# Kernel tuning notes

Measured on AMD Instinct MI355X. Metric: run time of the kernel, lower is better.

The kernel has to match this reference:

```python
import jax, jax.numpy as jnp
import numpy as np

N = 100000       # nodes
E = 3200000      # edges (avg degree 32)
C_IN = 32        # input_channels


def _glorot(key, shape):
    lim = float(np.sqrt(6.0 / (shape[0] + shape[1])))
    return jax.random.uniform(key, shape, jnp.float32, -lim, lim)


def setup_inputs() -> dict:
    key = jax.random.key(0)
    ks = jax.random.split(key, 8)
    x = jax.random.normal(ks[0], (N, C_IN), jnp.float32)
    edge_index = jax.random.randint(ks[1], (2, E), 0, N, dtype=jnp.int64)
    return {
        "x": x,
        "edge_index": edge_index,
        "W1": _glorot(ks[2], (C_IN, 16)), "b1": jnp.zeros((16,), jnp.float32),
        "W2": _glorot(ks[3], (16, 32)),   "b2": jnp.zeros((32,), jnp.float32),
        "W3": _glorot(ks[4], (32, 16)),   "b3": jnp.zeros((16,), jnp.float32),
        "Wfc": _glorot(ks[5], (16, 1)),   "bfc": jnp.zeros((1,), jnp.float32),
    }


def _gcn_conv(x, W, b, src, dst, norm, n):
    # PyG GCNConv: transform then degree-normalized scatter-add (self-loops in src/dst)
    h = x @ W                              # [N, out]
    m = h[src] * norm[:, None]             # gather + per-edge scale
    return jax.ops.segment_sum(m, dst, num_segments=n) + b


def reference(x, edge_index, W1, b1, W2, b2, W3, b3, Wfc, bfc):
    n = x.shape[0]
    loops = jnp.arange(n, dtype=edge_index.dtype)
    src = jnp.concatenate([edge_index[0], loops])   # add self-loops
    dst = jnp.concatenate([edge_index[1], loops])
    deg = jax.ops.segment_sum(jnp.ones(src.shape[0], x.dtype), dst, num_segments=n)
    dis = jnp.where(deg > 0, jax.lax.rsqrt(deg), jnp.zeros((), x.dtype))
    norm = dis[src] * dis[dst]                      # symmetric D^-1/2 A D^-1/2

    h = jax.nn.relu(_gcn_conv(x, W1, b1, src, dst, norm, n))
    h = jax.nn.relu(_gcn_conv(h, W2, b2, src, dst, norm, n))
    h = jax.nn.relu(_gcn_conv(h, W3, b3, src, dst, norm, n))
    out = h @ Wfc + bfc                             # [N, 1]
    return jnp.mean(out)
```

## Files before the change

### kernel.cpp

```cpp
#include <hip/hip_runtime.h>

static constexpr int BLK = 256;
static constexpr int CHUNK = 4096;
static constexpr int BSHIFT = 7;
static constexpr int BNODES = 128;
static constexpr int MAXNB = 1024;

typedef unsigned short bf16t;

__device__ __forceinline__ float bf_lo(unsigned u) { return __uint_as_float(u << 16); }
__device__ __forceinline__ float bf_hi(unsigned u) { return __uint_as_float(u & 0xFFFF0000u); }
__device__ __forceinline__ unsigned bf_r(float f) {
    unsigned x = __float_as_uint(f);
    x += 0x7fffu + ((x >> 16) & 1u);
    return x >> 16;
}
__device__ __forceinline__ unsigned bf_pack(float lo, float hi) {
    return bf_r(lo) | (bf_r(hi) << 16);
}


__global__ __launch_bounds__(BLK) void k_hist(const int* __restrict__ dst, int* __restrict__ ghist,
                                              int e, int NB, int NBLK) {
    __shared__ int h[MAXNB];
    for (int i = threadIdx.x; i < NB; i += BLK) h[i] = 0;
    __syncthreads();
    int base = blockIdx.x * CHUNK;
    int lim = min(e - base, CHUNK);
    for (int r = threadIdx.x; r < lim; r += BLK) atomicAdd(&h[dst[base + r] >> BSHIFT], 1);
    __syncthreads();
    for (int b = threadIdx.x; b < NB; b += BLK) ghist[b * NBLK + blockIdx.x] = h[b];
}

__global__ void k_scan1(const int* __restrict__ in, int* __restrict__ excl,
                        int* __restrict__ partials, int n) {
    __shared__ int s[BLK];
    int i = blockIdx.x * BLK + threadIdx.x;
    int v = (i < n) ? in[i] : 0;
    s[threadIdx.x] = v;
    __syncthreads();
    for (int off = 1; off < BLK; off <<= 1) {
        int t = ((int)threadIdx.x >= off) ? s[threadIdx.x - off] : 0;
        __syncthreads();
        s[threadIdx.x] += t;
        __syncthreads();
    }
    if (i < n) excl[i] = s[threadIdx.x] - v;
    if (threadIdx.x == BLK - 1) partials[blockIdx.x] = s[BLK - 1];
}

__global__ void k_scan2(int* __restrict__ partials, int P) {
    __shared__ int s[1024];
    int carry = 0;
    for (int base = 0; base < P; base += 1024) {
        int i = base + (int)threadIdx.x;
        int v = (i < P) ? partials[i] : 0;
        s[threadIdx.x] = v;
        __syncthreads();
        for (int off = 1; off < 1024; off <<= 1) {
            int t = ((int)threadIdx.x >= off) ? s[threadIdx.x - off] : 0;
            __syncthreads();
            s[threadIdx.x] += t;
            __syncthreads();
        }
        if (i < P) partials[i] = carry + s[threadIdx.x] - v;
        carry += s[1023];
        __syncthreads();
    }
}

__global__ void k_scan3(int* __restrict__ excl, const int* __restrict__ partials, int n) {
    int i = blockIdx.x * BLK + threadIdx.x;
    if (i < n) excl[i] += partials[blockIdx.x];
}

__global__ __launch_bounds__(BLK) void k_bin(const int* __restrict__ src, const int* __restrict__ dst,
                                             const int* __restrict__ goff, unsigned int* __restrict__ keys,
                                             int e, int NB, int NBLK) {
    __shared__ int hcur[MAXNB];
    __shared__ int sstart[MAXNB + 1];
    __shared__ unsigned int stage[CHUNK];
    __shared__ unsigned short bkt[CHUNK];
    for (int i = threadIdx.x; i < NB; i += BLK) hcur[i] = 0;
    __syncthreads();
    int base = blockIdx.x * CHUNK;
    int lim = min(e - base, CHUNK);
    for (int r = threadIdx.x; r < lim; r += BLK) atomicAdd(&hcur[dst[base + r] >> BSHIFT], 1);
    __syncthreads();
    for (int i = threadIdx.x; i < MAXNB; i += BLK) sstart[i] = (i < NB) ? hcur[i] : 0;
    __syncthreads();
    for (int off = 1; off < MAXNB; off <<= 1) {
        int tv[MAXNB / BLK];
#pragma unroll
        for (int j = 0; j < MAXNB / BLK; ++j) {
            int i = (int)threadIdx.x + j * BLK;
            tv[j] = (i >= off) ? sstart[i - off] : 0;
        }
        __syncthreads();
#pragma unroll
        for (int j = 0; j < MAXNB / BLK; ++j) sstart[(int)threadIdx.x + j * BLK] += tv[j];
        __syncthreads();
    }
    int ex[MAXNB / BLK];
#pragma unroll
    for (int j = 0; j < MAXNB / BLK; ++j) {
        int i = (int)threadIdx.x + j * BLK;
        ex[j] = sstart[i] - ((i < NB) ? hcur[i] : 0);
    }
    __syncthreads();
#pragma unroll
    for (int j = 0; j < MAXNB / BLK; ++j) {
        int i = (int)threadIdx.x + j * BLK;
        sstart[i] = ex[j];
        if (i < NB) hcur[i] = ex[j];
    }
    __syncthreads();
    for (int r = threadIdx.x; r < lim; r += BLK) {
        int s = src[base + r], d = dst[base + r];
        int b = d >> BSHIFT;
        int pos = atomicAdd(&hcur[b], 1);
        stage[pos] = (unsigned)s | ((unsigned)(d & (BNODES - 1)) << 20);
        bkt[pos] = (unsigned short)b;
    }
    __syncthreads();
    for (int j = threadIdx.x; j < lim; j += BLK) {
        int b = bkt[j];
        keys[goff[b * NBLK + blockIdx.x] + (j - sstart[b])] = stage[j];
    }
}

__global__ __launch_bounds__(BLK) void k_sortb(const unsigned int* __restrict__ keys,
                                               const int* __restrict__ goff,
                                               unsigned int* __restrict__ sorted,
                                               int* __restrict__ node_off, float* __restrict__ dis,
                                               int n, int NB, int NBLK, int e) {
    __shared__ int cnt[BNODES];
    __shared__ int sc[BNODES];
    __shared__ int cur[BNODES];
    int b = blockIdx.x;
    int start = goff[b * NBLK];
    int end = (b + 1 < NB) ? goff[(b + 1) * NBLK] : e;
    if (threadIdx.x < BNODES) cnt[threadIdx.x] = 0;
    __syncthreads();
    for (int k = start + (int)threadIdx.x; k < end; k += BLK) atomicAdd(&cnt[keys[k] >> 20], 1);
    __syncthreads();
    if (threadIdx.x < BNODES) sc[threadIdx.x] = cnt[threadIdx.x];
    __syncthreads();
    for (int off = 1; off < BNODES; off <<= 1) {
        int v = ((int)threadIdx.x < BNODES && (int)threadIdx.x >= off) ? sc[threadIdx.x - off] : 0;
        __syncthreads();
        if ((int)threadIdx.x < BNODES) sc[threadIdx.x] += v;
        __syncthreads();
    }
    if ((int)threadIdx.x < BNODES) {
        int excl = sc[threadIdx.x] - cnt[threadIdx.x];
        cur[threadIdx.x] = start + excl;
        int d = b * BNODES + (int)threadIdx.x;
        if (d < n) {
            node_off[d] = start + excl;
            dis[d] = rsqrtf(1.0f + (float)cnt[threadIdx.x]);
        }
    }
    if (b == NB - 1 && threadIdx.x == 0) node_off[n] = e;
    __syncthreads();
    for (int k = start + (int)threadIdx.x; k < end; k += BLK) {
        unsigned key = keys[k];
        int pos = atomicAdd(&cur[key >> 20], 1);
        sorted[pos] = key & 0xFFFFFu;
    }
}


template <int CIN, int COUT, bool BIAS, bool RELU_OUT, bool SCALE_OUT>
__global__ void k_transform(const float* __restrict__ in, const float* __restrict__ W,
                            const float* __restrict__ bias, const float* __restrict__ dis,
                            float* __restrict__ out, int n) {
    int t = blockIdx.x * BLK + threadIdx.x;
    int node = t / COUT, c = t % COUT;
    if (node >= n) return;
    const float* row = in + (size_t)node * CIN;
    float acc = BIAS ? bias[c] : 0.0f;
#pragma unroll
    for (int k = 0; k < CIN; ++k) acc = fmaf(row[k], W[k * COUT + c], acc);
    if (RELU_OUT) acc = fmaxf(acc, 0.0f);
    if (SCALE_OUT) acc *= dis[node];
    out[t] = acc;
}

__global__ void k_transform1_bf(const float* __restrict__ in, const float* __restrict__ W,
                                const float* __restrict__ dis, unsigned* __restrict__ out, int n) {
    int t = blockIdx.x * BLK + threadIdx.x;
    int node = t >> 3, j = t & 7;
    if (node >= n) return;
    const float* row = in + (size_t)node * 32;
    float a0 = 0.0f, a1 = 0.0f;
#pragma unroll
    for (int k = 0; k < 32; ++k) {
        float v = row[k];
        a0 = fmaf(v, W[k * 16 + 2 * j], a0);
        a1 = fmaf(v, W[k * 16 + 2 * j + 1], a1);
    }
    float sd = dis[node];
    out[t] = bf_pack(a0 * sd, a1 * sd);
}

template <int WMODE>
__global__ __launch_bounds__(BLK) void k_agg(const unsigned* __restrict__ in, const float* __restrict__ dis,
                                             const float* __restrict__ bias,
                                             const float* __restrict__ W2, const float* __restrict__ b2,
                                             const float* __restrict__ W3,
                                             const float* __restrict__ Wfc, const float* __restrict__ bfc,
                                             const unsigned int* __restrict__ sorted,
                                             const int* __restrict__ node_off,
                                             void* __restrict__ outv, int n) {
    int t = blockIdx.x * BLK + threadIdx.x;
    int d = t >> 3, j = t & 7;
    bool valid = d < n;
    int dd = valid ? d : 0;
    int k = node_off[dd], end = node_off[dd + 1];
    if (!valid) end = k;
    unsigned ws = valid ? in[((size_t)dd << 3) + j] : 0u;
    float l0 = bf_lo(ws), h0 = bf_hi(ws);
    float l1 = 0.0f, l2 = 0.0f, l3 = 0.0f, h1 = 0.0f, h2v = 0.0f, h3v = 0.0f;
    for (; k + 7 < end; k += 8) {
        int s0 = sorted[k],     s1 = sorted[k + 1], s2 = sorted[k + 2], s3 = sorted[k + 3];
        int s4 = sorted[k + 4], s5 = sorted[k + 5], s6 = sorted[k + 6], s7 = sorted[k + 7];
        unsigned w0 = in[((size_t)s0 << 3) + j];
        unsigned w1 = in[((size_t)s1 << 3) + j];
        unsigned w2 = in[((size_t)s2 << 3) + j];
        unsigned w3 = in[((size_t)s3 << 3) + j];
        unsigned w4 = in[((size_t)s4 << 3) + j];
        unsigned w5 = in[((size_t)s5 << 3) + j];
        unsigned w6 = in[((size_t)s6 << 3) + j];
        unsigned w7 = in[((size_t)s7 << 3) + j];
        l0 += bf_lo(w0) + bf_lo(w4);
        l1 += bf_lo(w1) + bf_lo(w5);
        l2 += bf_lo(w2) + bf_lo(w6);
        l3 += bf_lo(w3) + bf_lo(w7);
        h0 += bf_hi(w0) + bf_hi(w4);
        h1 += bf_hi(w1) + bf_hi(w5);
        h2v += bf_hi(w2) + bf_hi(w6);
        h3v += bf_hi(w3) + bf_hi(w7);
    }
    for (; k < end; ++k) {
        unsigned w = in[((size_t)sorted[k] << 3) + j];
        l0 += bf_lo(w);
        h0 += bf_hi(w);
    }
    float sd = dis[dd];
    float alo = ((l0 + l1) + (l2 + l3)) * sd;
    float ahi = ((h0 + h1) + (h2v + h3v)) * sd;

    if (WMODE == 0) {
        unsigned* out = (unsigned*)outv;
        if (valid)
            out[((size_t)d << 3) + j] =
                bf_pack(sd * fmaxf(bias[2 * j] + alo, 0.0f), sd * fmaxf(bias[2 * j + 1] + ahi, 0.0f));
    } else if (WMODE == 1) {
        float hh[4];
#pragma unroll
        for (int p = 0; p < 4; ++p) hh[p] = b2[j + 8 * p];
#pragma unroll
        for (int kk = 0; kk < 8; ++kk) {
            float rk0 = __shfl(alo, kk, 8);
            float rk1 = __shfl(ahi, kk, 8);
#pragma unroll
            for (int p = 0; p < 4; ++p) {
                hh[p] = fmaf(rk0, W2[(2 * kk) * 32 + j + 8 * p], hh[p]);
                hh[p] = fmaf(rk1, W2[(2 * kk + 1) * 32 + j + 8 * p], hh[p]);
            }
        }
#pragma unroll
        for (int p = 0; p < 4; ++p) hh[p] = fmaxf(hh[p], 0.0f);
        float zlo = 0.0f, zhi = 0.0f;
#pragma unroll
        for (int kk = 0; kk < 8; ++kk) {
#pragma unroll
            for (int p = 0; p < 4; ++p) {
                float u = __shfl(hh[p], kk, 8);
                zlo = fmaf(u, W3[(kk + 8 * p) * 16 + 2 * j], zlo);
                zhi = fmaf(u, W3[(kk + 8 * p) * 16 + 2 * j + 1], zhi);
            }
        }
        unsigned* out = (unsigned*)outv;
        if (valid) out[((size_t)d << 3) + j] = bf_pack(zlo * sd, zhi * sd);
    } else {
        float* partials = (float*)outv;
        float contrib = 0.0f;
        if (valid) {
            contrib = fmaf(fmaxf(bias[2 * j] + alo, 0.0f), Wfc[2 * j],
                           fmaf(fmaxf(bias[2 * j + 1] + ahi, 0.0f), Wfc[2 * j + 1], bfc[0] * 0.125f));
        }
#pragma unroll
        for (int m = 1; m < 64; m <<= 1) contrib += __shfl_xor(contrib, m, 64);
        __shared__ float sw[BLK / 64];
        if ((threadIdx.x & 63) == 0) sw[threadIdx.x >> 6] = contrib;
        __syncthreads();
        if (threadIdx.x == 0) {
            float tt = 0.0f;
#pragma unroll
            for (int w = 0; w < BLK / 64; ++w) tt += sw[w];
            partials[blockIdx.x] = tt;
        }
    }
}

__global__ __launch_bounds__(BLK) void k_reduce(const float* __restrict__ partials, int P,
                                                float* __restrict__ out, float inv_n) {
    float v = 0.0f;
    for (int i = threadIdx.x; i < P; i += BLK) v += partials[i];
#pragma unroll
    for (int m = 1; m < 64; m <<= 1) v += __shfl_xor(v, m, 64);
    __shared__ float sw[BLK / 64];
    if ((threadIdx.x & 63) == 0) sw[threadIdx.x >> 6] = v;
    __syncthreads();
    if (threadIdx.x == 0) {
        float tt = 0.0f;
#pragma unroll
        for (int w = 0; w < BLK / 64; ++w) tt += sw[w];
        out[0] = tt * inv_n;
    }
}


__global__ void k_deg_init(float* __restrict__ deg, int n) {
    int i = blockIdx.x * BLK + threadIdx.x;
    if (i < n) deg[i] = 1.0f;
}
__global__ void k_deg_count(const int* __restrict__ dst, float* __restrict__ deg, int e) {
    int i = blockIdx.x * BLK + threadIdx.x;
    if (i < e) atomicAdd(&deg[dst[i]], 1.0f);
}
__global__ void k_deg_rsqrt(float* __restrict__ deg, int n) {
    int i = blockIdx.x * BLK + threadIdx.x;
    if (i < n) deg[i] = rsqrtf(deg[i]);
}
template <int C, bool RELU_IN, bool BIAS>
__global__ void k_selfloop(const float* __restrict__ h, const float* __restrict__ dis,
                           const float* __restrict__ b, float* __restrict__ agg, int n) {
    int t = blockIdx.x * BLK + threadIdx.x;
    int node = t / C, c = t % C;
    if (node >= n) return;
    float w = dis[node];
    float v = h[t];
    if (RELU_IN) v = fmaxf(v, 0.0f);
    agg[t] = (BIAS ? b[c] : 0.0f) + v * w * w;
}
template <int C, bool RELU_IN>
__global__ void k_scatter(const int* __restrict__ src, const int* __restrict__ dst,
                          const float* __restrict__ h, const float* __restrict__ dis,
                          float* __restrict__ agg, int e) {
    int t = blockIdx.x * BLK + threadIdx.x;
    int edge = t / C, c = t % C;
    if (edge >= e) return;
    int s = src[edge], d = dst[edge];
    float w = dis[s] * dis[d];
    float v = h[(size_t)s * C + c];
    if (RELU_IN) v = fmaxf(v, 0.0f);
    atomicAdd(&agg[(size_t)d * C + c], v * w);
}
__global__ void k_zero(float* __restrict__ out) { out[0] = 0.0f; }
__global__ void k_final(const float* __restrict__ h, const float* __restrict__ Wfc,
                        const float* __restrict__ bfc, float* __restrict__ out, int n,
                        float inv_n) {
    int i = blockIdx.x * BLK + threadIdx.x;
    float v = 0.0f;
    if (i < n) {
        float acc = bfc[0];
        const float* row = h + (size_t)i * 16;
#pragma unroll
        for (int c = 0; c < 16; ++c) acc = fmaf(fmaxf(row[c], 0.0f), Wfc[c], acc);
        v = acc;
    }
#pragma unroll
    for (int off = 32; off > 0; off >>= 1) v += __shfl_down(v, off);
    __shared__ float sw[BLK / 64];
    int wid = threadIdx.x >> 6;
    if ((threadIdx.x & 63) == 0) sw[wid] = v;
    __syncthreads();
    if (threadIdx.x == 0) {
        float t = 0.0f;
#pragma unroll
        for (int w = 0; w < BLK / 64; ++w) t += sw[w];
        atomicAdd(out, t * inv_n);
    }
}


extern "C" void kernel_launch(void* const* d_in, const int* in_sizes, int n_in,
                              void* d_out, int out_size, void* d_ws, size_t ws_size,
                              hipStream_t stream) {
    const float* x   = (const float*)d_in[0];
    const int* ei    = (const int*)d_in[1];
    const float* W1  = (const float*)d_in[2];
    const float* b1  = (const float*)d_in[3];
    const float* W2  = (const float*)d_in[4];
    const float* b2  = (const float*)d_in[5];
    const float* W3  = (const float*)d_in[6];
    const float* b3  = (const float*)d_in[7];
    const float* Wfc = (const float*)d_in[8];
    const float* bfc = (const float*)d_in[9];
    float* out = (float*)d_out;

    const int n = in_sizes[0] / 32;
    const int e = in_sizes[1] / 2;
    const int* src = ei;
    const int* dst = ei + e;

    auto g1 = [](long long work) { return dim3((unsigned)((work + BLK - 1) / BLK)); };

    const int NB   = (n + BNODES - 1) >> BSHIFT;
    const int NBLK = (e + CHUNK - 1) / CHUNK;
    const long long L = (long long)NB * NBLK;
    const int P = (int)((L + BLK - 1) / BLK);
    const int PM = (int)(((long long)n * 8 + BLK - 1) / BLK);

    auto align_up = [](size_t v) { return (v + 255) & ~(size_t)255; };
    size_t off = 0;
    auto carve = [&](size_t bytes) { size_t o = off; off += align_up(bytes); return o; };
    char* base = (char*)d_ws;
    size_t o_dis   = carve((size_t)n * 4);
    size_t o_noff  = carve(((size_t)n + 1) * 4);
    size_t o_ghist = carve((size_t)L * 4);
    size_t o_goff  = carve((size_t)L * 4);
    size_t o_part  = carve(((size_t)P + 1) * 4);
    size_t o_pm    = carve((size_t)PM * 4);
    size_t o_A     = carve((size_t)n * 16 * 2);
    size_t o_B     = carve((size_t)n * 16 * 2);
    size_t o_keys  = carve((size_t)e * 4);
    size_t o_sort  = carve((size_t)e * 4);
    bool ok = (off <= ws_size) && (NB <= MAXNB) && (n < (1 << 20));

    if (ok) {
        float* dis  = (float*)(base + o_dis);
        int* noff   = (int*)(base + o_noff);
        int* ghist  = (int*)(base + o_ghist);
        int* goff   = (int*)(base + o_goff);
        int* part   = (int*)(base + o_part);
        float* pm   = (float*)(base + o_pm);
        unsigned* A = (unsigned*)(base + o_A);
        unsigned* B = (unsigned*)(base + o_B);
        unsigned int* keys   = (unsigned int*)(base + o_keys);
        unsigned int* sorted = (unsigned int*)(base + o_sort);

        k_hist<<<dim3(NBLK), BLK, 0, stream>>>(dst, ghist, e, NB, NBLK);
        k_scan1<<<g1(L), BLK, 0, stream>>>(ghist, goff, part, (int)L);
        k_scan2<<<1, 1024, 0, stream>>>(part, P);
        k_scan3<<<g1(L), BLK, 0, stream>>>(goff, part, (int)L);
        k_bin<<<dim3(NBLK), BLK, 0, stream>>>(src, dst, goff, keys, e, NB, NBLK);
        k_sortb<<<dim3(NB), BLK, 0, stream>>>(keys, goff, sorted, noff, dis, n, NB, NBLK, e);

        k_transform1_bf<<<g1((long long)n * 8), BLK, 0, stream>>>(x, W1, dis, A, n);
        k_agg<0><<<g1((long long)n * 8), BLK, 0, stream>>>(A, dis, b1, nullptr, nullptr, nullptr, nullptr, nullptr,
                                                           sorted, noff, B, n);
        k_agg<1><<<g1((long long)n * 8), BLK, 0, stream>>>(B, dis, nullptr, W2, b2, W3, nullptr, nullptr,
                                                           sorted, noff, A, n);
        k_agg<2><<<g1((long long)n * 8), BLK, 0, stream>>>(A, dis, b3, nullptr, nullptr, nullptr, Wfc, bfc,
                                                           sorted, noff, pm, n);
        k_reduce<<<1, BLK, 0, stream>>>(pm, PM, out, 1.0f / (float)n);
    } else {
        float* dis = (float*)d_ws;
        float* A = dis + (((size_t)n + 255) & ~(size_t)255);
        float* B = A + (size_t)n * 32;

        k_deg_init<<<g1(n), BLK, 0, stream>>>(dis, n);
        k_deg_count<<<g1(e), BLK, 0, stream>>>(dst, dis, e);
        k_deg_rsqrt<<<g1(n), BLK, 0, stream>>>(dis, n);

        k_transform<32, 16, false, false, false><<<g1((long long)n * 16), BLK, 0, stream>>>(x, W1, nullptr, nullptr, A, n);
        k_selfloop<16, false, true><<<g1((long long)n * 16), BLK, 0, stream>>>(A, dis, b1, B, n);
        k_scatter<16, false><<<g1((long long)e * 16), BLK, 0, stream>>>(src, dst, A, dis, B, e);

        k_selfloop<16, true, false><<<g1((long long)n * 16), BLK, 0, stream>>>(B, dis, nullptr, A, n);
        k_scatter<16, true><<<g1((long long)e * 16), BLK, 0, stream>>>(src, dst, B, dis, A, e);
        k_transform<16, 32, true, true, false><<<g1((long long)n * 32), BLK, 0, stream>>>(A, W2, b2, nullptr, B, n);

        k_transform<32, 16, false, false, false><<<g1((long long)n * 16), BLK, 0, stream>>>(B, W3, nullptr, nullptr, A, n);
        k_selfloop<16, false, true><<<g1((long long)n * 16), BLK, 0, stream>>>(A, dis, b3, B, n);
        k_scatter<16, false><<<g1((long long)e * 16), BLK, 0, stream>>>(src, dst, A, dis, B, e);

        k_zero<<<1, 1, 0, stream>>>(out);
        k_final<<<g1(n), BLK, 0, stream>>>(B, Wfc, bfc, out, n, 1.0f / (float)n);
    }
}
```

Measured before the change: 193.7 us.

## Vectorize edge loads in binning/sort and use 4 lanes per node in aggregation

The histogram, binning and bucket-sort kernels now read dst/src/keys as int4/uint4 when the chunk is aligned, with scalar head and tail loops. The aggregation kernels switch from 8 lanes per node with 32-bit loads to 4 lanes per node with 64-bit (uint2) bf16 loads and vectorized index reads. The fused W2/W3 shuffle transform and the final partial-sum reduction are reworked to match. This halves the thread count and per-gather instruction count, at the cost of more registers per thread and fewer threads hiding gather latency.

After: 186.9 us. -3.6%, faster.

```diff
diff --git a/kernel.cpp b/kernel.cpp
--- a/kernel.cpp
+++ b/kernel.cpp
@@ -5,8 +5,6 @@
 static constexpr int BSHIFT = 7;
 static constexpr int BNODES = 128;
 static constexpr int MAXNB = 1024;
-
-typedef unsigned short bf16t;
 
 __device__ __forceinline__ float bf_lo(unsigned u) { return __uint_as_float(u << 16); }
 __device__ __forceinline__ float bf_hi(unsigned u) { return __uint_as_float(u & 0xFFFF0000u); }
@@ -27,7 +25,19 @@
     __syncthreads();
     int base = blockIdx.x * CHUNK;
     int lim = min(e - base, CHUNK);
-    for (int r = threadIdx.x; r < lim; r += BLK) atomicAdd(&h[dst[base + r] >> BSHIFT], 1);
+    bool v4 = ((((size_t)(dst + base)) & 15) == 0);
+    if (v4 && lim == CHUNK) {
+        const int4* d4 = (const int4*)(dst + base);
+        for (int q = threadIdx.x; q < CHUNK / 4; q += BLK) {
+            int4 v = d4[q];
+            atomicAdd(&h[v.x >> BSHIFT], 1);
+            atomicAdd(&h[v.y >> BSHIFT], 1);
+            atomicAdd(&h[v.z >> BSHIFT], 1);
+            atomicAdd(&h[v.w >> BSHIFT], 1);
+        }
+    } else {
+        for (int r = threadIdx.x; r < lim; r += BLK) atomicAdd(&h[dst[base + r] >> BSHIFT], 1);
+    }
     __syncthreads();
     for (int b = threadIdx.x; b < NB; b += BLK) ghist[b * NBLK + blockIdx.x] = h[b];
 }
@@ -85,7 +95,19 @@
     __syncthreads();
     int base = blockIdx.x * CHUNK;
     int lim = min(e - base, CHUNK);
-    for (int r = threadIdx.x; r < lim; r += BLK) atomicAdd(&hcur[dst[base + r] >> BSHIFT], 1);
+    bool v4 = ((((size_t)(dst + base)) & 15) == 0) && ((((size_t)(src + base)) & 15) == 0) && (lim == CHUNK);
+    if (v4) {
+        const int4* d4 = (const int4*)(dst + base);
+        for (int q = threadIdx.x; q < CHUNK / 4; q += BLK) {
+            int4 v = d4[q];
+            atomicAdd(&hcur[v.x >> BSHIFT], 1);
+            atomicAdd(&hcur[v.y >> BSHIFT], 1);
+            atomicAdd(&hcur[v.z >> BSHIFT], 1);
+            atomicAdd(&hcur[v.w >> BSHIFT], 1);
+        }
+    } else {
+        for (int r = threadIdx.x; r < lim; r += BLK) atomicAdd(&hcur[dst[base + r] >> BSHIFT], 1);
+    }
     __syncthreads();
     for (int i = threadIdx.x; i < MAXNB; i += BLK) sstart[i] = (i < NB) ? hcur[i] : 0;
     __syncthreads();
@@ -115,12 +137,30 @@
         if (i < NB) hcur[i] = ex[j];
     }
     __syncthreads();
-    for (int r = threadIdx.x; r < lim; r += BLK) {
-        int s = src[base + r], d = dst[base + r];
-        int b = d >> BSHIFT;
-        int pos = atomicAdd(&hcur[b], 1);
-        stage[pos] = (unsigned)s | ((unsigned)(d & (BNODES - 1)) << 20);
-        bkt[pos] = (unsigned short)b;
+    if (v4) {
+        const int4* s4 = (const int4*)(src + base);
+        const int4* d4 = (const int4*)(dst + base);
+        for (int q = threadIdx.x; q < CHUNK / 4; q += BLK) {
+            int4 sv = s4[q];
+            int4 dv = d4[q];
+#pragma unroll
+            for (int u = 0; u < 4; ++u) {
+                int s = (u == 0) ? sv.x : (u == 1) ? sv.y : (u == 2) ? sv.z : sv.w;
+                int d = (u == 0) ? dv.x : (u == 1) ? dv.y : (u == 2) ? dv.z : dv.w;
+                int b = d >> BSHIFT;
+                int pos = atomicAdd(&hcur[b], 1);
+                stage[pos] = (unsigned)s | ((unsigned)(d & (BNODES - 1)) << 20);
+                bkt[pos] = (unsigned short)b;
+            }
+        }
+    } else {
+        for (int r = threadIdx.x; r < lim; r += BLK) {
+            int s = src[base + r], d = dst[base + r];
+            int b = d >> BSHIFT;
+            int pos = atomicAdd(&hcur[b], 1);
+            stage[pos] = (unsigned)s | ((unsigned)(d & (BNODES - 1)) << 20);
+            bkt[pos] = (unsigned short)b;
+        }
     }
     __syncthreads();
     for (int j = threadIdx.x; j < lim; j += BLK) {
@@ -142,7 +182,21 @@
     int end = (b + 1 < NB) ? goff[(b + 1) * NBLK] : e;
     if (threadIdx.x < BNODES) cnt[threadIdx.x] = 0;
     __syncthreads();
-    for (int k = start + (int)threadIdx.x; k < end; k += BLK) atomicAdd(&cnt[keys[k] >> 20], 1);
+    int astart = (start + 3) & ~3;
+    if (astart > end) astart = end;
+    int nq = (end - astart) >> 2;
+    for (int k = start + (int)threadIdx.x; k < astart; k += BLK) atomicAdd(&cnt[keys[k] >> 20], 1);
+    {
+        const uint4* k4 = (const uint4*)(keys + astart);
+        for (int q = threadIdx.x; q < nq; q += BLK) {
+            uint4 v = k4[q];
+            atomicAdd(&cnt[v.x >> 20], 1);
+            atomicAdd(&cnt[v.y >> 20], 1);
+            atomicAdd(&cnt[v.z >> 20], 1);
+            atomicAdd(&cnt[v.w >> 20], 1);
+        }
+    }
+    for (int k = astart + (nq << 2) + (int)threadIdx.x; k < end; k += BLK) atomicAdd(&cnt[keys[k] >> 20], 1);
     __syncthreads();
     if (threadIdx.x < BNODES) sc[threadIdx.x] = cnt[threadIdx.x];
     __syncthreads();
@@ -163,7 +217,24 @@
     }
     if (b == NB - 1 && threadIdx.x == 0) node_off[n] = e;
     __syncthreads();
-    for (int k = start + (int)threadIdx.x; k < end; k += BLK) {
+    for (int k = start + (int)threadIdx.x; k < astart; k += BLK) {
+        unsigned key = keys[k];
+        int pos = atomicAdd(&cur[key >> 20], 1);
+        sorted[pos] = key & 0xFFFFFu;
+    }
+    {
+        const uint4* k4 = (const uint4*)(keys + astart);
+        for (int q = threadIdx.x; q < nq; q += BLK) {
+            uint4 v = k4[q];
+#pragma unroll
+            for (int u = 0; u < 4; ++u) {
+                unsigned key = (u == 0) ? v.x : (u == 1) ? v.y : (u == 2) ? v.z : v.w;
+                int pos = atomicAdd(&cur[key >> 20], 1);
+                sorted[pos] = key & 0xFFFFFu;
+            }
+        }
+    }
+    for (int k = astart + (nq << 2) + (int)threadIdx.x; k < end; k += BLK) {
         unsigned key = keys[k];
         int pos = atomicAdd(&cur[key >> 20], 1);
         sorted[pos] = key & 0xFFFFFu;
@@ -214,82 +285,108 @@
                                              const int* __restrict__ node_off,
                                              void* __restrict__ outv, int n) {
     int t = blockIdx.x * BLK + threadIdx.x;
-    int d = t >> 3, j = t & 7;
+    int d = t >> 2, j = t & 3;
     bool valid = d < n;
     int dd = valid ? d : 0;
     int k = node_off[dd], end = node_off[dd + 1];
     if (!valid) end = k;
-    unsigned ws = valid ? in[((size_t)dd << 3) + j] : 0u;
-    float l0 = bf_lo(ws), h0 = bf_hi(ws);
-    float l1 = 0.0f, l2 = 0.0f, l3 = 0.0f, h1 = 0.0f, h2v = 0.0f, h3v = 0.0f;
+    const uint2* inrow = (const uint2*)in;
+    uint2 zz; zz.x = 0u; zz.y = 0u;
+    uint2 ws = valid ? inrow[((size_t)dd << 2) + j] : zz;
+    float a00 = bf_lo(ws.x), a10 = bf_hi(ws.x), a20 = bf_lo(ws.y), a30 = bf_hi(ws.y);
+    float a01 = 0.0f, a11 = 0.0f, a21 = 0.0f, a31 = 0.0f;
+    for (; k < end && (k & 3); ++k) {
+        uint2 w = inrow[((size_t)sorted[k] << 2) + j];
+        a00 += bf_lo(w.x); a10 += bf_hi(w.x); a20 += bf_lo(w.y); a30 += bf_hi(w.y);
+    }
     for (; k + 7 < end; k += 8) {
-        int s0 = sorted[k],     s1 = sorted[k + 1], s2 = sorted[k + 2], s3 = sorted[k + 3];
-        int s4 = sorted[k + 4], s5 = sorted[k + 5], s6 = sorted[k + 6], s7 = sorted[k + 7];
-        unsigned w0 = in[((size_t)s0 << 3) + j];
-        unsigned w1 = in[((size_t)s1 << 3) + j];
-        unsigned w2 = in[((size_t)s2 << 3) + j];
-        unsigned w3 = in[((size_t)s3 << 3) + j];
-        unsigned w4 = in[((size_t)s4 << 3) + j];
-        unsigned w5 = in[((size_t)s5 << 3) + j];
-        unsigned w6 = in[((size_t)s6 << 3) + j];
-        unsigned w7 = in[((size_t)s7 << 3) + j];
-        l0 += bf_lo(w0) + bf_lo(w4);
-        l1 += bf_lo(w1) + bf_lo(w5);
-        l2 += bf_lo(w2) + bf_lo(w6);
-        l3 += bf_lo(w3) + bf_lo(w7);
-        h0 += bf_hi(w0) + bf_hi(w4);
-        h1 += bf_hi(w1) + bf_hi(w5);
-        h2v += bf_hi(w2) + bf_hi(w6);
-        h3v += bf_hi(w3) + bf_hi(w7);
+        uint4 i0 = *(const uint4*)(sorted + k);
+        uint4 i1 = *(const uint4*)(sorted + k + 4);
+        uint2 w0 = inrow[((size_t)i0.x << 2) + j];
+        uint2 w1 = inrow[((size_t)i0.y << 2) + j];
+        uint2 w2 = inrow[((size_t)i0.z << 2) + j];
+        uint2 w3 = inrow[((size_t)i0.w << 2) + j];
+        uint2 w4 = inrow[((size_t)i1.x << 2) + j];
+        uint2 w5 = inrow[((size_t)i1.y << 2) + j];
+        uint2 w6 = inrow[((size_t)i1.z << 2) + j];
+        uint2 w7 = inrow[((size_t)i1.w << 2) + j];
+        a00 += (bf_lo(w0.x) + bf_lo(w2.x)) + (bf_lo(w4.x) + bf_lo(w6.x));
+        a01 += (bf_lo(w1.x) + bf_lo(w3.x)) + (bf_lo(w5.x) + bf_lo(w7.x));
+        a10 += (bf_hi(w0.x) + bf_hi(w2.x)) + (bf_hi(w4.x) + bf_hi(w6.x));
+        a11 += (bf_hi(w1.x) + bf_hi(w3.x)) + (bf_hi(w5.x) + bf_hi(w7.x));
+        a20 += (bf_lo(w0.y) + bf_lo(w2.y)) + (bf_lo(w4.y) + bf_lo(w6.y));
+        a21 += (bf_lo(w1.y) + bf_lo(w3.y)) + (bf_lo(w5.y) + bf_lo(w7.y));
+        a30 += (bf_hi(w0.y) + bf_hi(w2.y)) + (bf_hi(w4.y) + bf_hi(w6.y));
+        a31 += (bf_hi(w1.y) + bf_hi(w3.y)) + (bf_hi(w5.y) + bf_hi(w7.y));
     }
     for (; k < end; ++k) {
-        unsigned w = in[((size_t)sorted[k] << 3) + j];
-        l0 += bf_lo(w);
-        h0 += bf_hi(w);
+        uint2 w = inrow[((size_t)sorted[k] << 2) + j];
+        a00 += bf_lo(w.x); a10 += bf_hi(w.x); a20 += bf_lo(w.y); a30 += bf_hi(w.y);
     }
     float sd = dis[dd];
-    float alo = ((l0 + l1) + (l2 + l3)) * sd;
-    float ahi = ((h0 + h1) + (h2v + h3v)) * sd;
+    float a0 = (a00 + a01) * sd;
+    float a1 = (a10 + a11) * sd;
+    float a2 = (a20 + a21) * sd;
+    float a3 = (a30 + a31) * sd;
 
     if (WMODE == 0) {
-        unsigned* out = (unsigned*)outv;
-        if (valid)
-            out[((size_t)d << 3) + j] =
-                bf_pack(sd * fmaxf(bias[2 * j] + alo, 0.0f), sd * fmaxf(bias[2 * j + 1] + ahi, 0.0f));
+        uint2* out = (uint2*)outv;
+        if (valid) {
+            uint2 r;
+            r.x = bf_pack(sd * fmaxf(bias[4 * j] + a0, 0.0f), sd * fmaxf(bias[4 * j + 1] + a1, 0.0f));
+            r.y = bf_pack(sd * fmaxf(bias[4 * j + 2] + a2, 0.0f), sd * fmaxf(bias[4 * j + 3] + a3, 0.0f));
+            out[((size_t)d << 2) + j] = r;
+        }
     } else if (WMODE == 1) {
-        float hh[4];
-#pragma unroll
-        for (int p = 0; p < 4; ++p) hh[p] = b2[j + 8 * p];
-#pragma unroll
-        for (int kk = 0; kk < 8; ++kk) {
-            float rk0 = __shfl(alo, kk, 8);
-            float rk1 = __shfl(ahi, kk, 8);
-#pragma unroll
-            for (int p = 0; p < 4; ++p) {
-                hh[p] = fmaf(rk0, W2[(2 * kk) * 32 + j + 8 * p], hh[p]);
-                hh[p] = fmaf(rk1, W2[(2 * kk + 1) * 32 + j + 8 * p], hh[p]);
+        float hh[8];
+#pragma unroll
+        for (int p = 0; p < 8; ++p) hh[p] = b2[j + 4 * p];
+#pragma unroll
+        for (int kk = 0; kk < 4; ++kk) {
+            float r0 = __shfl(a0, kk, 4);
+            float r1 = __shfl(a1, kk, 4);
+            float r2 = __shfl(a2, kk, 4);
+            float r3 = __shfl(a3, kk, 4);
+#pragma unroll
+            for (int p = 0; p < 8; ++p) {
+                int m = j + 4 * p;
+                hh[p] = fmaf(r0, W2[(4 * kk) * 32 + m], hh[p]);
+                hh[p] = fmaf(r1, W2[(4 * kk + 1) * 32 + m], hh[p]);
+                hh[p] = fmaf(r2, W2[(4 * kk + 2) * 32 + m], hh[p]);
+                hh[p] = fmaf(r3, W2[(4 * kk + 3) * 32 + m], hh[p]);
             }
         }
 #pragma unroll
-        for (int p = 0; p < 4; ++p) hh[p] = fmaxf(hh[p], 0.0f);
-        float zlo = 0.0f, zhi = 0.0f;
-#pragma unroll
-        for (int kk = 0; kk < 8; ++kk) {
-#pragma unroll
-            for (int p = 0; p < 4; ++p) {
-                float u = __shfl(hh[p], kk, 8);
-                zlo = fmaf(u, W3[(kk + 8 * p) * 16 + 2 * j], zlo);
-                zhi = fmaf(u, W3[(kk + 8 * p) * 16 + 2 * j + 1], zhi);
+        for (int p = 0; p < 8; ++p) hh[p] = fmaxf(hh[p], 0.0f);
+        float z0 = 0.0f, z1 = 0.0f, z2 = 0.0f, z3 = 0.0f;
+#pragma unroll
+        for (int kk = 0; kk < 4; ++kk) {
+#pragma unroll
+            for (int p = 0; p < 8; ++p) {
+                float u = __shfl(hh[p], kk, 4);
+                int m = kk + 4 * p;
+                z0 = fmaf(u, W3[m * 16 + 4 * j], z0);
+                z1 = fmaf(u, W3[m * 16 + 4 * j + 1], z1);
+                z2 = fmaf(u, W3[m * 16 + 4 * j + 2], z2);
+                z3 = fmaf(u, W3[m * 16 + 4 * j + 3], z3);
             }
         }
-        unsigned* out = (unsigned*)outv;
-        if (valid) out[((size_t)d << 3) + j] = bf_pack(zlo * sd, zhi * sd);
+        uint2* out = (uint2*)outv;
+        if (valid) {
+            uint2 r;
+            r.x = bf_pack(z0 * sd, z1 * sd);
+            r.y = bf_pack(z2 * sd, z3 * sd);
+            out[((size_t)d << 2) + j] = r;
+        }
     } else {
         float* partials = (float*)outv;
         float contrib = 0.0f;
         if (valid) {
-            contrib = fmaf(fmaxf(bias[2 * j] + alo, 0.0f), Wfc[2 * j],
-                           fmaf(fmaxf(bias[2 * j + 1] + ahi, 0.0f), Wfc[2 * j + 1], bfc[0] * 0.125f));
+            contrib = bfc[0] * 0.25f;
+            contrib = fmaf(fmaxf(bias[4 * j] + a0, 0.0f), Wfc[4 * j], contrib);
+            contrib = fmaf(fmaxf(bias[4 * j + 1] + a1, 0.0f), Wfc[4 * j + 1], contrib);
+            contrib = fmaf(fmaxf(bias[4 * j + 2] + a2, 0.0f), Wfc[4 * j + 2], contrib);
+            contrib = fmaf(fmaxf(bias[4 * j + 3] + a3, 0.0f), Wfc[4 * j + 3], contrib);
         }
 #pragma unroll
         for (int m = 1; m < 64; m <<= 1) contrib += __shfl_xor(contrib, m, 64);
@@ -413,7 +510,7 @@
     const int NBLK = (e + CHUNK - 1) / CHUNK;
     const long long L = (long long)NB * NBLK;
     const int P = (int)((L + BLK - 1) / BLK);
-    const int PM = (int)(((long long)n * 8 + BLK - 1) / BLK);
+    const int PM = (int)(((long long)n * 4 + BLK - 1) / BLK);
 
     auto align_up = [](size_t v) { return (v + 255) & ~(size_t)255; };
     size_t off = 0;
@@ -451,11 +548,11 @@
         k_sortb<<<dim3(NB), BLK, 0, stream>>>(keys, goff, sorted, noff, dis, n, NB, NBLK, e);
 
         k_transform1_bf<<<g1((long long)n * 8), BLK, 0, stream>>>(x, W1, dis, A, n);
-        k_agg<0><<<g1((long long)n * 8), BLK, 0, stream>>>(A, dis, b1, nullptr, nullptr, nullptr, nullptr, nullptr,
+        k_agg<0><<<g1((long long)n * 4), BLK, 0, stream>>>(A, dis, b1, nullptr, nullptr, nullptr, nullptr, nullptr,
                                                            sorted, noff, B, n);
-        k_agg<1><<<g1((long long)n * 8), BLK, 0, stream>>>(B, dis, nullptr, W2, b2, W3, nullptr, nullptr,
+        k_agg<1><<<g1((long long)n * 4), BLK, 0, stream>>>(B, dis, nullptr, W2, b2, W3, nullptr, nullptr,
                                                            sorted, noff, A, n);
-        k_agg<2><<<g1((long long)n * 8), BLK, 0, stream>>>(A, dis, b3, nullptr, nullptr, nullptr, Wfc, bfc,
+        k_agg<2><<<g1((long long)n * 4), BLK, 0, stream>>>(A, dis, b3, nullptr, nullptr, nullptr, Wfc, bfc,
                                                            sorted, noff, pm, n);
         k_reduce<<<1, BLK, 0, stream>>>(pm, PM, out, 1.0f / (float)n);
     } else {
```
